# Kernel optimization log

Hardware: AMD Instinct MI355X
Metric: run time of the kernel (lower is better)

Reference implementation:

```python
import jax, jax.numpy as jnp
import numpy as np

N = 16777216  # batch*A*width*height (flat anchor-score vector)
BINS = 10
LOSS_WEIGHT = 1.0


def setup_inputs() -> dict:
    key = jax.random.key(0)
    k1, k2, k3 = jax.random.split(key, 3)
    pred = jax.random.normal(k1, (N,), dtype=jnp.float32)          # IoU logits
    target = jax.random.uniform(k2, (N,), dtype=jnp.float32)       # IoU targets in [0,1]
    label_weight = (jax.random.uniform(k3, (N,)) > 0.3).astype(jnp.float32)  # 1=valid, 0=ignore
    return {"pred": pred, "target": target, "label_weight": label_weight, "bins": BINS}


def reference(pred, target, label_weight, bins):
    # target is detached in the original module
    target = jax.lax.stop_gradient(target)
    # gradient norm g = |sigmoid(pred).detach() - target|, lies in [0,1]
    g = jnp.abs(jax.lax.stop_gradient(jax.nn.sigmoid(pred)) - target)
    valid = label_weight > 0
    validf = valid.astype(jnp.float32)
    tot = jnp.maximum(jnp.sum(validf), 1.0)

    # edges are i/bins with last edge nudged by 1e-6, so bin = floor(g*bins) clipped to bins-1
    bin_idx = jnp.clip((g * bins).astype(jnp.int32), 0, bins - 1)
    counts = jax.ops.segment_sum(validf, bin_idx, num_segments=bins)  # per-bin valid counts
    n = jnp.sum(counts > 0).astype(jnp.float32)                        # number of nonempty bins
    counts_safe = jnp.maximum(counts, 1.0)
    w_per_bin = jnp.where(counts > 0, tot / counts_safe, 0.0) / jnp.maximum(n, 1.0)
    weights = jnp.where(valid, w_per_bin[bin_idx], 0.0)

    # weighted BCE-with-logits, reduction='sum', stable form: logaddexp(0,x) - x*z
    bce = jnp.logaddexp(0.0, pred) - pred * target
    loss = jnp.sum(weights * bce) / tot
    return loss * LOSS_WEIGHT
```

## Files before the change

### kernel.cpp

```cpp
#include <hip/hip_runtime.h>

#define BINS 10
#define REPLICAS 32

__global__ __launch_bounds__(256, 4)
void ghm_pass1(const float* __restrict__ pred,
               const float* __restrict__ target,
               const float* __restrict__ lw,
               float* __restrict__ rep_sums,
               unsigned int* __restrict__ rep_cnts,
               int n)
{
    __shared__ float ls[BINS];
    __shared__ unsigned int lc[BINS];
    if (threadIdx.x < BINS) { ls[threadIdx.x] = 0.0f; lc[threadIdx.x] = 0u; }
    __syncthreads();

    float s[BINS];
    unsigned int c[BINS];
#pragma unroll
    for (int b = 0; b < BINS; ++b) { s[b] = 0.0f; c[b] = 0u; }

    auto process = [&](float p, float t, float w) {
        float sig = 1.0f / (1.0f + __expf(-p));
        float g = fabsf(sig - t);
        int bi = (int)(g * (float)BINS);
        bi = bi > (BINS - 1) ? (BINS - 1) : bi;
        float bce = fmaxf(p, 0.0f) + log1pf(__expf(-fabsf(p))) - p * t;
        bool valid = w > 0.0f;
#pragma unroll
        for (int b = 0; b < BINS; ++b) {
            bool hit = valid && (bi == b);
            c[b] += hit ? 1u : 0u;
            s[b] += hit ? bce : 0.0f;
        }
    };

    const int gid = blockIdx.x * blockDim.x + threadIdx.x;
    const int stride = gridDim.x * blockDim.x;
    const int n4 = n >> 2;
    const float4* p4 = (const float4*)pred;
    const float4* t4 = (const float4*)target;
    const float4* w4 = (const float4*)lw;
    for (int i = gid; i < n4; i += stride) {
        float4 pv = p4[i];
        float4 tv = t4[i];
        float4 wv = w4[i];
        process(pv.x, tv.x, wv.x);
        process(pv.y, tv.y, wv.y);
        process(pv.z, tv.z, wv.z);
        process(pv.w, tv.w, wv.w);
    }
    for (int i = (n4 << 2) + gid; i < n; i += stride) {
        process(pred[i], target[i], lw[i]);
    }

    const int lane = threadIdx.x & 63;
#pragma unroll
    for (int b = 0; b < BINS; ++b) {
        float v = s[b];
        unsigned int cc = c[b];
#pragma unroll
        for (int off = 32; off > 0; off >>= 1) {
            v += __shfl_down(v, off, 64);
            cc += __shfl_down(cc, off, 64);
        }
        if (lane == 0) {
            atomicAdd(&ls[b], v);
            atomicAdd(&lc[b], cc);
        }
    }
    __syncthreads();
    if (threadIdx.x < BINS) {
        int rep = (int)(blockIdx.x & (REPLICAS - 1));
        atomicAdd(&rep_sums[rep * BINS + threadIdx.x], ls[threadIdx.x]);
        atomicAdd(&rep_cnts[rep * BINS + threadIdx.x], lc[threadIdx.x]);
    }
}

__global__ void ghm_finalize(const float* __restrict__ rep_sums,
                             const unsigned int* __restrict__ rep_cnts,
                             float* __restrict__ out)
{
    __shared__ double S[BINS];
    __shared__ unsigned int C[BINS];
    int t = threadIdx.x;
    if (t < BINS) {
        double s = 0.0;
        unsigned int cc = 0u;
        for (int r = 0; r < REPLICAS; ++r) {
            s += (double)rep_sums[r * BINS + t];
            cc += rep_cnts[r * BINS + t];
        }
        S[t] = s;
        C[t] = cc;
    }
    __syncthreads();
    if (t == 0) {
        double n = 0.0;
        for (int b = 0; b < BINS; ++b)
            if (C[b] > 0u) n += 1.0;
        double nn = n > 1.0 ? n : 1.0;
        double loss = 0.0;
        for (int b = 0; b < BINS; ++b)
            if (C[b] > 0u) loss += S[b] / ((double)C[b] * nn);
        out[0] = (float)loss;
    }
}

extern "C" void kernel_launch(void* const* d_in, const int* in_sizes, int n_in,
                              void* d_out, int out_size, void* d_ws, size_t ws_size,
                              hipStream_t stream)
{
    const float* pred = (const float*)d_in[0];
    const float* target = (const float*)d_in[1];
    const float* lw = (const float*)d_in[2];
    int n = in_sizes[0];

    float* rep_sums = (float*)d_ws;
    unsigned int* rep_cnts =
        (unsigned int*)((char*)d_ws + REPLICAS * BINS * sizeof(float));

    hipMemsetAsync(d_ws, 0,
                   REPLICAS * BINS * (sizeof(float) + sizeof(unsigned int)),
                   stream);
    ghm_pass1<<<2048, 256, 0, stream>>>(pred, target, lw, rep_sums, rep_cnts, n);
    ghm_finalize<<<1, 64, 0, stream>>>(rep_sums, rep_cnts, (float*)d_out);
}
```

Baseline: 217.3 us.

## Fuse finalize into main kernel via last-block counter and use fast exp/log intrinsics

Merges the finalize kernel into the main pass. A global done counter lets the last block sum the per-replica bin partials and write the loss, which removes one kernel launch. It also rewrites the sigmoid and softplus to share a single exp2 of -|p|, using hardware rcp/log builtins, and folds the validity mask into an out-of-range bin index. Replicas are halved to 16, and the final sum now runs in float shared atomics instead of double, which slightly changes accumulation order and precision.

```diff
diff --git a/kernel.cpp b/kernel.cpp
--- a/kernel.cpp
+++ b/kernel.cpp
@@ -1,43 +1,51 @@
 #include <hip/hip_runtime.h>
 
 #define BINS 10
-#define REPLICAS 32
+#define REPLICAS 16
+#define NBLOCKS 2048
+#define NTHREADS 256
 
-__global__ __launch_bounds__(256, 4)
-void ghm_pass1(const float* __restrict__ pred,
+
+__global__ __launch_bounds__(NTHREADS, 4)
+void ghm_fused(const float* __restrict__ pred,
                const float* __restrict__ target,
                const float* __restrict__ lw,
                float* __restrict__ rep_sums,
                unsigned int* __restrict__ rep_cnts,
+               unsigned int* __restrict__ done_ctr,
+               float* __restrict__ out,
                int n)
 {
     __shared__ float ls[BINS];
     __shared__ unsigned int lc[BINS];
+    __shared__ unsigned int isLast;
     if (threadIdx.x < BINS) { ls[threadIdx.x] = 0.0f; lc[threadIdx.x] = 0u; }
-    __syncthreads();
 
-    float s[BINS];
-    unsigned int c[BINS];
-#pragma unroll
-    for (int b = 0; b < BINS; ++b) { s[b] = 0.0f; c[b] = 0u; }
+    float s0=0.f,s1=0.f,s2=0.f,s3=0.f,s4=0.f,s5=0.f,s6=0.f,s7=0.f,s8=0.f,s9=0.f;
+    unsigned int c0=0,c1=0,c2=0,c3=0,c4=0,c5=0,c6=0,c7=0,c8=0,c9=0;
 
-    auto process = [&](float p, float t, float w) {
-        float sig = 1.0f / (1.0f + __expf(-p));
-        float g = fabsf(sig - t);
-        int bi = (int)(g * (float)BINS);
-        bi = bi > (BINS - 1) ? (BINS - 1) : bi;
-        float bce = fmaxf(p, 0.0f) + log1pf(__expf(-fabsf(p))) - p * t;
-        bool valid = w > 0.0f;
-#pragma unroll
-        for (int b = 0; b < BINS; ++b) {
-            bool hit = valid && (bi == b);
-            c[b] += hit ? 1u : 0u;
-            s[b] += hit ? bce : 0.0f;
-        }
-    };
+#define BINACC(B, S, C) { bool h_ = (bi_ == (B)); (C) += h_ ? 1u : 0u; (S) += h_ ? bce_ : 0.0f; }
 
-    const int gid = blockIdx.x * blockDim.x + threadIdx.x;
-    const int stride = gridDim.x * blockDim.x;
+#define PROC(P, T, W) do {                                                     \
+    float p_ = (P), t_ = (T);                                                  \
+    float ap_ = fabsf(p_);                                                     \
+    float q_  = __builtin_amdgcn_exp2f(ap_ * -1.4426950408889634f); \
+    float r_  = __builtin_amdgcn_rcpf(1.0f + q_);                              \
+    float sig_ = (p_ >= 0.0f) ? r_ : (1.0f - r_);              \
+    float g_   = fabsf(sig_ - t_);                                             \
+    int bi_ = (int)(g_ * 10.0f);                                               \
+    bi_ = bi_ > 9 ? 9 : bi_;                                                   \
+    bi_ = ((W) > 0.0f) ? bi_ : 15;                      \
+    float bce_ = fmaxf(p_, 0.0f)                                               \
+               + 0.6931471805599453f * __builtin_amdgcn_logf(1.0f + q_)        \
+               - p_ * t_;                                                      \
+    BINACC(0,s0,c0) BINACC(1,s1,c1) BINACC(2,s2,c2) BINACC(3,s3,c3)            \
+    BINACC(4,s4,c4) BINACC(5,s5,c5) BINACC(6,s6,c6) BINACC(7,s7,c7)            \
+    BINACC(8,s8,c8) BINACC(9,s9,c9)                                            \
+} while (0)
+
+    const int gid = blockIdx.x * NTHREADS + threadIdx.x;
+    const int stride = NBLOCKS * NTHREADS;
     const int n4 = n >> 2;
     const float4* p4 = (const float4*)pred;
     const float4* t4 = (const float4*)target;
@@ -46,66 +54,77 @@
         float4 pv = p4[i];
         float4 tv = t4[i];
         float4 wv = w4[i];
-        process(pv.x, tv.x, wv.x);
-        process(pv.y, tv.y, wv.y);
-        process(pv.z, tv.z, wv.z);
-        process(pv.w, tv.w, wv.w);
+        PROC(pv.x, tv.x, wv.x);
+        PROC(pv.y, tv.y, wv.y);
+        PROC(pv.z, tv.z, wv.z);
+        PROC(pv.w, tv.w, wv.w);
     }
     for (int i = (n4 << 2) + gid; i < n; i += stride) {
-        process(pred[i], target[i], lw[i]);
+        PROC(pred[i], target[i], lw[i]);
     }
 
-    const int lane = threadIdx.x & 63;
-#pragma unroll
-    for (int b = 0; b < BINS; ++b) {
-        float v = s[b];
-        unsigned int cc = c[b];
-#pragma unroll
-        for (int off = 32; off > 0; off >>= 1) {
-            v += __shfl_down(v, off, 64);
-            cc += __shfl_down(cc, off, 64);
-        }
-        if (lane == 0) {
-            atomicAdd(&ls[b], v);
-            atomicAdd(&lc[b], cc);
-        }
+#define WREDUCE(S, C) {                                                        \
+    _Pragma("unroll")                                                          \
+    for (int o_ = 32; o_ > 0; o_ >>= 1) {                                      \
+        (S) += __shfl_down((S), o_, 64);                                       \
+        (C) += __shfl_down((C), o_, 64);                                       \
+    } }
+    WREDUCE(s0,c0) WREDUCE(s1,c1) WREDUCE(s2,c2) WREDUCE(s3,c3) WREDUCE(s4,c4)
+    WREDUCE(s5,c5) WREDUCE(s6,c6) WREDUCE(s7,c7) WREDUCE(s8,c8) WREDUCE(s9,c9)
+
+    __syncthreads();
+    if ((threadIdx.x & 63) == 0) {
+        atomicAdd(&ls[0], s0); atomicAdd(&lc[0], c0);
+        atomicAdd(&ls[1], s1); atomicAdd(&lc[1], c1);
+        atomicAdd(&ls[2], s2); atomicAdd(&lc[2], c2);
+        atomicAdd(&ls[3], s3); atomicAdd(&lc[3], c3);
+        atomicAdd(&ls[4], s4); atomicAdd(&lc[4], c4);
+        atomicAdd(&ls[5], s5); atomicAdd(&lc[5], c5);
+        atomicAdd(&ls[6], s6); atomicAdd(&lc[6], c6);
+        atomicAdd(&ls[7], s7); atomicAdd(&lc[7], c7);
+        atomicAdd(&ls[8], s8); atomicAdd(&lc[8], c8);
+        atomicAdd(&ls[9], s9); atomicAdd(&lc[9], c9);
     }
     __syncthreads();
     if (threadIdx.x < BINS) {
-        int rep = (int)(blockIdx.x & (REPLICAS - 1));
+        int rep = blockIdx.x & (REPLICAS - 1);
         atomicAdd(&rep_sums[rep * BINS + threadIdx.x], ls[threadIdx.x]);
         atomicAdd(&rep_cnts[rep * BINS + threadIdx.x], lc[threadIdx.x]);
     }
-}
-
-__global__ void ghm_finalize(const float* __restrict__ rep_sums,
-                             const unsigned int* __restrict__ rep_cnts,
-                             float* __restrict__ out)
-{
-    __shared__ double S[BINS];
-    __shared__ unsigned int C[BINS];
-    int t = threadIdx.x;
-    if (t < BINS) {
-        double s = 0.0;
-        unsigned int cc = 0u;
-        for (int r = 0; r < REPLICAS; ++r) {
-            s += (double)rep_sums[r * BINS + t];
-            cc += rep_cnts[r * BINS + t];
-        }
-        S[t] = s;
-        C[t] = cc;
+    __syncthreads();
+    if (threadIdx.x == 0) {
+        __threadfence();
+        unsigned int old = atomicAdd(done_ctr, 1u);
+        isLast = (old == (unsigned int)(NBLOCKS - 1)) ? 1u : 0u;
     }
     __syncthreads();
-    if (t == 0) {
-        double n = 0.0;
-        for (int b = 0; b < BINS; ++b)
-            if (C[b] > 0u) n += 1.0;
-        double nn = n > 1.0 ? n : 1.0;
-        double loss = 0.0;
-        for (int b = 0; b < BINS; ++b)
-            if (C[b] > 0u) loss += S[b] / ((double)C[b] * nn);
-        out[0] = (float)loss;
+
+    if (isLast) {
+        __threadfence();
+        if (threadIdx.x < BINS) { ls[threadIdx.x] = 0.0f; lc[threadIdx.x] = 0u; }
+        __syncthreads();
+        if (threadIdx.x < REPLICAS * BINS) {
+            float sv = __hip_atomic_load(&rep_sums[threadIdx.x],
+                                         __ATOMIC_RELAXED, __HIP_MEMORY_SCOPE_AGENT);
+            unsigned int cv = __hip_atomic_load(&rep_cnts[threadIdx.x],
+                                               __ATOMIC_RELAXED, __HIP_MEMORY_SCOPE_AGENT);
+            atomicAdd(&ls[threadIdx.x % BINS], sv);
+            atomicAdd(&lc[threadIdx.x % BINS], cv);
+        }
+        __syncthreads();
+        if (threadIdx.x == 0) {
+            double n_ne = 0.0;
+            for (int b = 0; b < BINS; ++b) if (lc[b] > 0u) n_ne += 1.0;
+            double nn = n_ne > 1.0 ? n_ne : 1.0;
+            double loss = 0.0;
+            for (int b = 0; b < BINS; ++b)
+                if (lc[b] > 0u) loss += (double)ls[b] / ((double)lc[b] * nn);
+            out[0] = (float)loss;
+        }
     }
+#undef PROC
+#undef BINACC
+#undef WREDUCE
 }
 
 extern "C" void kernel_launch(void* const* d_in, const int* in_sizes, int n_in,
@@ -118,12 +137,12 @@
     int n = in_sizes[0];
 
     float* rep_sums = (float*)d_ws;
-    unsigned int* rep_cnts =
-        (unsigned int*)((char*)d_ws + REPLICAS * BINS * sizeof(float));
+    unsigned int* rep_cnts = (unsigned int*)((char*)d_ws + REPLICAS * BINS * sizeof(float));
+    unsigned int* done_ctr = (unsigned int*)((char*)d_ws + 2 * REPLICAS * BINS * sizeof(float));
 
-    hipMemsetAsync(d_ws, 0,
-                   REPLICAS * BINS * (sizeof(float) + sizeof(unsigned int)),
+    hipMemsetAsync(d_ws, 0, 2 * REPLICAS * BINS * sizeof(float) + sizeof(unsigned int),
                    stream);
-    ghm_pass1<<<2048, 256, 0, stream>>>(pred, target, lw, rep_sums, rep_cnts, n);
-    ghm_finalize<<<1, 64, 0, stream>>>(rep_sums, rep_cnts, (float*)d_out);
+    ghm_fused<<<NBLOCKS, NTHREADS, 0, stream>>>(pred, target, lw, rep_sums,
+                                                rep_cnts, done_ctr,
+                                                (float*)d_out, n);
 }
```

After: 301.1 us. 1.39x slower.
